# Optimization experiments

Hardware: AMD Instinct MI355X
Metric: run time of the kernel (lower is better)

Reference implementation:

```python
import jax, jax.numpy as jnp
import numpy as np

N_NODES = 200000
N_EDGES = 800000
N_GRAPHS = 4096
ATOM_DIM = 128
HIDDEN = 256
LN_EPS = 1e-5


def _layer_norm(x, g, b):
    m = jnp.mean(x, axis=-1, keepdims=True)
    v = jnp.mean((x - m) ** 2, axis=-1, keepdims=True)
    return (x - m) / jnp.sqrt(v + LN_EPS) * g + b


def setup_inputs() -> dict:
    key = jax.random.key(0)
    ks = jax.random.split(key, 16)
    d = {}
    d['x'] = jax.random.normal(ks[0], (N_NODES, ATOM_DIM), dtype=jnp.float32)
    d['edge_index'] = jax.random.randint(ks[1], (2, N_EDGES), 0, N_NODES, dtype=jnp.int32)
    # sorted batch assignment covering all graphs (PyG batches are sorted)
    d['batch'] = ((jnp.arange(N_NODES) * N_GRAPHS) // N_NODES).astype(jnp.int32)

    def glorot(k, shape):
        fan_in, fan_out = shape[0], shape[1]
        s = jnp.sqrt(2.0 / (fan_in + fan_out))
        return jax.random.normal(k, shape, dtype=jnp.float32) * s

    d['gin1_w1'] = glorot(ks[2], (ATOM_DIM, HIDDEN)); d['gin1_b1'] = jnp.zeros((HIDDEN,), jnp.float32)
    d['gin1_w2'] = glorot(ks[3], (HIDDEN, HIDDEN));  d['gin1_b2'] = jnp.zeros((HIDDEN,), jnp.float32)
    d['gin2_w1'] = glorot(ks[4], (HIDDEN, HIDDEN));  d['gin2_b1'] = jnp.zeros((HIDDEN,), jnp.float32)
    d['gin2_w2'] = glorot(ks[5], (HIDDEN, HIDDEN));  d['gin2_b2'] = jnp.zeros((HIDDEN,), jnp.float32)
    d['ln_g'] = jnp.ones((HIDDEN,), jnp.float32);    d['ln_b'] = jnp.zeros((HIDDEN,), jnp.float32)
    d['s2_w1'] = glorot(ks[6], (HIDDEN, 768));       d['s2_b1'] = jnp.zeros((768,), jnp.float32)
    d['s2_ln_g'] = jnp.ones((768,), jnp.float32);    d['s2_ln_b'] = jnp.zeros((768,), jnp.float32)
    d['s2_w2'] = glorot(ks[7], (768, 2));            d['s2_b2'] = jnp.zeros((2,), jnp.float32)
    return d


def reference(x, edge_index, batch,
              gin1_w1, gin1_b1, gin1_w2, gin1_b2,
              gin2_w1, gin2_b1, gin2_w2, gin2_b2,
              ln_g, ln_b,
              s2_w1, s2_b1, s2_ln_g, s2_ln_b, s2_w2, s2_b2):
    src, dst = edge_index[0], edge_index[1]

    def gin_conv(h, w1, b1, w2, b2):
        # GINConv: mlp((1+eps)*x + sum_{j in N(i)} x_j), eps=0
        agg = jax.ops.segment_sum(h[src], dst, num_segments=h.shape[0])
        z = h + agg
        return jax.nn.relu(z @ w1 + b1) @ w2 + b2

    h = gin_conv(x, gin1_w1, gin1_b1, gin1_w2, gin1_b2)
    h = jax.nn.leaky_relu(_layer_norm(h, ln_g, ln_b), 0.2)
    h = gin_conv(h, gin2_w1, gin2_b1, gin2_w2, gin2_b2)
    h = jax.nn.leaky_relu(h, 0.2)
    # global max pool over graphs
    g = jax.ops.segment_max(h, batch, num_segments=N_GRAPHS)
    # seq2 head (dropout = identity in eval)
    z = jax.nn.leaky_relu(_layer_norm(g @ s2_w1 + s2_b1, s2_ln_g, s2_ln_b), 0.2)
    z = z @ s2_w2 + s2_b2
    return jax.nn.softmax(z, axis=-1)
```

## Files before the change

### kernel.cpp

```cpp
#include <hip/hip_runtime.h>

#define NN 200000
#define NE 800000
#define NG 4096
#define AD 128
#define HD 256
#define LN_EPS 1e-5f
#define NB 782

typedef __attribute__((ext_vector_type(8))) short     bf16x8;
typedef __attribute__((ext_vector_type(8))) unsigned short us8;
typedef __attribute__((ext_vector_type(4))) unsigned short us4;
typedef __attribute__((ext_vector_type(4))) float     f32x4;

typedef __attribute__((address_space(1))) const unsigned gl_t;
typedef __attribute__((address_space(3))) unsigned       ld_t;

__device__ __forceinline__ float leaky(float v){ return v > 0.f ? v : 0.2f*v; }

__device__ __forceinline__ unsigned short f2bf(float f){
  unsigned u = __float_as_uint(f);
  return (unsigned short)((u + 0x7FFFu + ((u >> 16) & 1u)) >> 16);
}
__device__ __forceinline__ float bf2f(unsigned short h){ return __uint_as_float(((unsigned)h) << 16); }

__device__ __forceinline__ unsigned fkey(float f){
  unsigned u = __float_as_uint(f);
  return (u & 0x80000000u) ? ~u : (u | 0x80000000u);
}
__device__ __forceinline__ float fdec(unsigned k){
  return (k & 0x80000000u) ? __uint_as_float(k & 0x7FFFFFFFu) : __uint_as_float(~k);
}

__global__ __launch_bounds__(256) void k_zero(int* __restrict__ cur){
  int i = blockIdx.x * 256 + threadIdx.x;
  if (i < NN) cur[i] = 0;
}

__global__ __launch_bounds__(256) void k_count(const int* __restrict__ ei, int* __restrict__ cur){
  int e = blockIdx.x * 256 + threadIdx.x;
  atomicAdd(&cur[ei[NE + e]], 1);
}

__global__ __launch_bounds__(256) void k_scanA(const int* __restrict__ cur, int* __restrict__ partial){
  __shared__ int sd[256];
  int t = threadIdx.x, b = blockIdx.x, i = b * 256 + t;
  sd[t] = (i < NN) ? cur[i] : 0;
  __syncthreads();
  for (int off = 128; off >= 1; off >>= 1){
    if (t < off) sd[t] += sd[t + off];
    __syncthreads();
  }
  if (t == 0) partial[b] = sd[0];
}

__global__ __launch_bounds__(1024) void k_scanB(const int* __restrict__ partial,
                                                int* __restrict__ scanoff, int* __restrict__ rowptr){
  __shared__ int sd[1024];
  int t = threadIdx.x;
  int v = (t < NB) ? partial[t] : 0;
  sd[t] = v; __syncthreads();
  for (int off = 1; off < 1024; off <<= 1){
    int u = (t >= off) ? sd[t - off] : 0;
    __syncthreads();
    sd[t] += u;
    __syncthreads();
  }
  if (t < NB) scanoff[t] = sd[t] - v;
  if (t == 0) rowptr[NN] = NE;
}

__global__ __launch_bounds__(256) void k_scanC(int* __restrict__ cur, const int* __restrict__ scanoff,
                                               int* __restrict__ rowptr){
  __shared__ int sd[256];
  int t = threadIdx.x, b = blockIdx.x, i = b * 256 + t;
  int v = (i < NN) ? cur[i] : 0;
  sd[t] = v; __syncthreads();
  for (int off = 1; off < 256; off <<= 1){
    int u = (t >= off) ? sd[t - off] : 0;
    __syncthreads();
    sd[t] += u;
    __syncthreads();
  }
  if (i < NN){ rowptr[i] = scanoff[b] + sd[t] - v; cur[i] = 0; }
}

__global__ __launch_bounds__(256) void k_fill(const int* __restrict__ ei,
                                              const int* __restrict__ rowptr,
                                              int* __restrict__ cur,
                                              int* __restrict__ col){
  int e = blockIdx.x * 256 + threadIdx.x;
  int s = ei[e], d = ei[NE + e];
  int pos = atomicAdd(&cur[d], 1);
  col[rowptr[d] + pos] = s;
}

__global__ __launch_bounds__(256) void k_initG(unsigned* __restrict__ Gk){
  int i = blockIdx.x * 256 + threadIdx.x;
  Gk[i] = 0x00800000u;
}

__global__ __launch_bounds__(256) void k_wprep(const float* __restrict__ src,
                                               unsigned short* __restrict__ dst, int K){
  int k = blockIdx.x, n = threadIdx.x;
  dst[(size_t)n * K + k] = f2bf(src[(size_t)k * 256 + n]);
}

__global__ __launch_bounds__(256) void k_layer1(const float* __restrict__ x,
                                                const int* __restrict__ rowptr,
                                                const int* __restrict__ col,
                                                const unsigned short* __restrict__ W1T,
                                                const float* __restrict__ b1,
                                                const unsigned short* __restrict__ W2T,
                                                const float* __restrict__ b2,
                                                const float* __restrict__ lng,
                                                const float* __restrict__ lnb,
                                                unsigned short* __restrict__ H1){
  __shared__ alignas(16) char gbuf[32768 + 4096];
  __shared__ float2 redS[16][4];
  char* zS = gbuf + 32768;
  char* tS = gbuf;
  const int tid = threadIdx.x;
  const int l = tid & 63, wv = tid >> 6;
  const int cl = l & 15, kg = l >> 4;
  const int row0 = blockIdx.x * 16;
  const int r16 = tid >> 4, sub = tid & 15;
  const int grow = row0 + r16;

  const float4* x4 = (const float4*)x;
  float a[8];
  {
    float4 s0 = x4[(size_t)grow * 32 + sub * 2];
    float4 s1 = x4[(size_t)grow * 32 + sub * 2 + 1];
    a[0]=s0.x; a[1]=s0.y; a[2]=s0.z; a[3]=s0.w; a[4]=s1.x; a[5]=s1.y; a[6]=s1.z; a[7]=s1.w;
  }
  const int pr = rowptr[grow], per = rowptr[grow + 1];
  const int p0 = rowptr[row0], pend = rowptr[row0 + 16];

  for (int cs = p0; cs < pend; cs += 64){
    const int ns = min(64, pend - cs);
    {
      const int cidx = cs + wv * 16 + (l & 15);
      int colv = (cidx < pend) ? col[cidx] : 0;
      #pragma unroll
      for (int i = 0; i < 8; ++i){
        const int lslot = wv * 16 + i * 2 + (l >> 5);
        const int j = __shfl(colv, i * 2 + (l >> 5));
        if (lslot < ns){
          const void* src = (const void*)(x + (size_t)j * AD + (l & 31) * 4);
          void* dst = (void*)(gbuf + (wv * 16 + i * 2) * 512);
          __builtin_amdgcn_global_load_lds((gl_t*)src, (ld_t*)dst, 16, 0, 0);
        }
      }
    }
    __syncthreads();
    {
      const int qlo = max(pr, cs), qhi = min(per, cs + ns);
      for (int q = qlo; q < qhi; ++q){
        const float4* lrow = (const float4*)(gbuf + (q - cs) * 512 + sub * 32);
        float4 c0 = lrow[0], c1 = lrow[1];
        a[0]+=c0.x; a[1]+=c0.y; a[2]+=c0.z; a[3]+=c0.w;
        a[4]+=c1.x; a[5]+=c1.y; a[6]+=c1.z; a[7]+=c1.w;
      }
    }
    __syncthreads();
  }

  {
    us8 o;
    #pragma unroll
    for (int j = 0; j < 8; ++j) o[j] = f2bf(a[j]);
    *(us8*)&zS[r16 * 256 + ((sub * 16) ^ ((r16 & 7) << 4))] = o;
  }
  __syncthreads();

  f32x4 acc[4];
  #pragma unroll
  for (int nt = 0; nt < 4; ++nt){
    float bv = b1[wv * 64 + nt * 16 + cl];
    acc[nt] = (f32x4){bv, bv, bv, bv};
  }
  #pragma unroll
  for (int ks = 0; ks < 4; ++ks){
    const int kb = (ks * 32 + kg * 8) * 2;
    bf16x8 a0 = *(const bf16x8*)&zS[cl * 256 + (kb ^ ((cl & 7) << 4))];
    #pragma unroll
    for (int nt = 0; nt < 4; ++nt){
      bf16x8 b = *(const bf16x8*)(W1T + (size_t)(wv * 64 + nt * 16 + cl) * AD + ks * 32 + kg * 8);
      acc[nt] = __builtin_amdgcn_mfma_f32_16x16x32_bf16(a0, b, acc[nt], 0, 0, 0);
    }
  }
  #pragma unroll
  for (int nt = 0; nt < 4; ++nt)
    #pragma unroll
    for (int rg = 0; rg < 4; ++rg){
      float v = fmaxf(acc[nt][rg], 0.f);
      int row = kg * 4 + rg;
      int cc = wv * 64 + nt * 16 + cl;
      *(unsigned short*)&tS[row * 512 + ((cc * 2) ^ ((row & 7) << 4))] = f2bf(v);
    }
  __syncthreads();

  #pragma unroll
  for (int nt = 0; nt < 4; ++nt){
    float bv = b2[wv * 64 + nt * 16 + cl];
    acc[nt] = (f32x4){bv, bv, bv, bv};
  }
  #pragma unroll
  for (int ks = 0; ks < 8; ++ks){
    const int kb = (ks * 32 + kg * 8) * 2;
    bf16x8 a0 = *(const bf16x8*)&tS[cl * 512 + (kb ^ ((cl & 7) << 4))];
    #pragma unroll
    for (int nt = 0; nt < 4; ++nt){
      bf16x8 b = *(const bf16x8*)(W2T + (size_t)(wv * 64 + nt * 16 + cl) * HD + ks * 32 + kg * 8);
      acc[nt] = __builtin_amdgcn_mfma_f32_16x16x32_bf16(a0, b, acc[nt], 0, 0, 0);
    }
  }

  float s1v[4], s2v[4];
  #pragma unroll
  for (int rg = 0; rg < 4; ++rg){
    float aa = acc[0][rg] + acc[1][rg] + acc[2][rg] + acc[3][rg];
    float bb = acc[0][rg]*acc[0][rg] + acc[1][rg]*acc[1][rg]
             + acc[2][rg]*acc[2][rg] + acc[3][rg]*acc[3][rg];
    #pragma unroll
    for (int off = 1; off <= 8; off <<= 1){ aa += __shfl_xor(aa, off); bb += __shfl_xor(bb, off); }
    s1v[rg] = aa; s2v[rg] = bb;
  }
  if (cl == 0){
    #pragma unroll
    for (int rg = 0; rg < 4; ++rg)
      redS[kg * 4 + rg][wv] = make_float2(s1v[rg], s2v[rg]);
  }
  __syncthreads();
  #pragma unroll
  for (int rg = 0; rg < 4; ++rg){
    int row = kg * 4 + rg;
    float t1 = redS[row][0].x + redS[row][1].x + redS[row][2].x + redS[row][3].x;
    float t2 = redS[row][0].y + redS[row][1].y + redS[row][2].y + redS[row][3].y;
    float m  = t1 * (1.f / HD);
    float vr = t2 * (1.f / HD) - m * m;
    float rs = rsqrtf(vr + LN_EPS);
    #pragma unroll
    for (int nt = 0; nt < 4; ++nt){
      int cc = wv * 64 + nt * 16 + cl;
      float v = (acc[nt][rg] - m) * rs * lng[cc] + lnb[cc];
      H1[(size_t)(row0 + row) * HD + cc] = f2bf(leaky(v));
    }
  }
}

__global__ __launch_bounds__(256) void k_layer2(const unsigned short* __restrict__ H1,
                                                const int* __restrict__ rowptr,
                                                const int* __restrict__ col,
                                                const int* __restrict__ batch,
                                                const unsigned short* __restrict__ W1T,
                                                const float* __restrict__ b1,
                                                const unsigned short* __restrict__ W2T,
                                                const float* __restrict__ b2,
                                                unsigned* __restrict__ Gk){
  __shared__ alignas(16) char gbuf[32768 + 8192];
  char* zS = gbuf + 32768;
  char* tS = gbuf;
  float* stageF = (float*)gbuf;
  const int tid = threadIdx.x;
  const int l = tid & 63, wv = tid >> 6;
  const int cl = l & 15, kg = l >> 4;
  const int row0 = blockIdx.x * 16;
  const int r16 = tid >> 4, sub = tid & 15;
  const int grow = row0 + r16;

  float a[16];
  {
    us8 a0 = *(const us8*)(H1 + (size_t)grow * HD + sub * 16);
    us8 a1 = *(const us8*)(H1 + (size_t)grow * HD + sub * 16 + 8);
    #pragma unroll
    for (int j = 0; j < 8; ++j){ a[j] = bf2f(a0[j]); a[8 + j] = bf2f(a1[j]); }
  }
  const int pr = rowptr[grow], per = rowptr[grow + 1];
  const int p0 = rowptr[row0], pend = rowptr[row0 + 16];

  for (int cs = p0; cs < pend; cs += 64){
    const int ns = min(64, pend - cs);
    {
      const int cidx = cs + wv * 16 + (l & 15);
      int colv = (cidx < pend) ? col[cidx] : 0;
      #pragma unroll
      for (int i = 0; i < 8; ++i){
        const int lslot = wv * 16 + i * 2 + (l >> 5);
        const int j = __shfl(colv, i * 2 + (l >> 5));
        if (lslot < ns){
          const void* src = (const void*)(H1 + (size_t)j * HD + (l & 31) * 8);
          void* dst = (void*)(gbuf + (wv * 16 + i * 2) * 512);
          __builtin_amdgcn_global_load_lds((gl_t*)src, (ld_t*)dst, 16, 0, 0);
        }
      }
    }
    __syncthreads();
    {
      const int qlo = max(pr, cs), qhi = min(per, cs + ns);
      for (int q = qlo; q < qhi; ++q){
        const us8* lrow = (const us8*)(gbuf + (q - cs) * 512 + sub * 32);
        us8 c0 = lrow[0], c1 = lrow[1];
        #pragma unroll
        for (int j = 0; j < 8; ++j){ a[j] += bf2f(c0[j]); a[8 + j] += bf2f(c1[j]); }
      }
    }
    __syncthreads();
  }

  {
    us8 o0, o1;
    #pragma unroll
    for (int j = 0; j < 8; ++j){ o0[j] = f2bf(a[j]); o1[j] = f2bf(a[8 + j]); }
    const int swz = (r16 & 7) << 4;
    *(us8*)&zS[r16 * 512 + ((sub * 32) ^ swz)]      = o0;
    *(us8*)&zS[r16 * 512 + ((sub * 32 + 16) ^ swz)] = o1;
  }
  __syncthreads();

  f32x4 acc[4];
  #pragma unroll
  for (int nt = 0; nt < 4; ++nt){
    float bv = b1[wv * 64 + nt * 16 + cl];
    acc[nt] = (f32x4){bv, bv, bv, bv};
  }
  #pragma unroll
  for (int ks = 0; ks < 8; ++ks){
    const int kb = (ks * 32 + kg * 8) * 2;
    bf16x8 a0 = *(const bf16x8*)&zS[cl * 512 + (kb ^ ((cl & 7) << 4))];
    #pragma unroll
    for (int nt = 0; nt < 4; ++nt){
      bf16x8 b = *(const bf16x8*)(W1T + (size_t)(wv * 64 + nt * 16 + cl) * HD + ks * 32 + kg * 8);
      acc[nt] = __builtin_amdgcn_mfma_f32_16x16x32_bf16(a0, b, acc[nt], 0, 0, 0);
    }
  }
  #pragma unroll
  for (int nt = 0; nt < 4; ++nt)
    #pragma unroll
    for (int rg = 0; rg < 4; ++rg){
      float v = fmaxf(acc[nt][rg], 0.f);
      int row = kg * 4 + rg;
      int cc = wv * 64 + nt * 16 + cl;
      *(unsigned short*)&tS[row * 512 + ((cc * 2) ^ ((row & 7) << 4))] = f2bf(v);
    }
  __syncthreads();

  #pragma unroll
  for (int nt = 0; nt < 4; ++nt){
    float bv = b2[wv * 64 + nt * 16 + cl];
    acc[nt] = (f32x4){bv, bv, bv, bv};
  }
  #pragma unroll
  for (int ks = 0; ks < 8; ++ks){
    const int kb = (ks * 32 + kg * 8) * 2;
    bf16x8 a0 = *(const bf16x8*)&tS[cl * 512 + (kb ^ ((cl & 7) << 4))];
    #pragma unroll
    for (int nt = 0; nt < 4; ++nt){
      bf16x8 b = *(const bf16x8*)(W2T + (size_t)(wv * 64 + nt * 16 + cl) * HD + ks * 32 + kg * 8);
      acc[nt] = __builtin_amdgcn_mfma_f32_16x16x32_bf16(a0, b, acc[nt], 0, 0, 0);
    }
  }
  __syncthreads();

  #pragma unroll
  for (int nt = 0; nt < 4; ++nt)
    #pragma unroll
    for (int rg = 0; rg < 4; ++rg){
      int row = kg * 4 + rg;
      int cc = wv * 64 + nt * 16 + cl;
      stageF[row * HD + cc] = leaky(acc[nt][rg]);
    }
  __syncthreads();

  {
    const int c = tid;
    int gprev = batch[row0];
    float m = -3.4e38f;
    #pragma unroll
    for (int r = 0; r < 16; ++r){
      int g = batch[row0 + r];
      if (g != gprev){
        atomicMax(&Gk[(size_t)gprev * HD + c], fkey(m));
        m = -3.4e38f;
        gprev = g;
      }
      m = fmaxf(m, stageF[r * HD + c]);
    }
    atomicMax(&Gk[(size_t)gprev * HD + c], fkey(m));
  }
}

__global__ __launch_bounds__(256) void head_kernel(const unsigned* __restrict__ Gk,
                                                   const float* __restrict__ w1,
                                                   const float* __restrict__ b1,
                                                   const float* __restrict__ lng,
                                                   const float* __restrict__ lnb,
                                                   const float* __restrict__ w2,
                                                   const float* __restrict__ b2,
                                                   float* __restrict__ out){
  __shared__ float gs[8][256];
  __shared__ float redA[8][4], redB[8][4];
  const int tid = threadIdx.x;
  const int g0 = blockIdx.x * 8;
  #pragma unroll
  for (int q = 0; q < 8; ++q) gs[q][tid] = fdec(Gk[(size_t)(g0 + q) * 256 + tid]);
  __syncthreads();

  float z[8][3];
  #pragma unroll
  for (int j = 0; j < 3; ++j){
    const int c = tid + j * 256;
    float a[8];
    float bv = b1[c];
    #pragma unroll
    for (int q = 0; q < 8; ++q) a[q] = bv;
    #pragma unroll 8
    for (int k = 0; k < 256; ++k){
      float w = w1[(size_t)k * 768 + c];
      #pragma unroll
      for (int q = 0; q < 8; ++q) a[q] += gs[q][k] * w;
    }
    #pragma unroll
    for (int q = 0; q < 8; ++q) z[q][j] = a[q];
  }

  const int lane = tid & 63, wv = tid >> 6;
  float mean[8], rs[8];
  {
    float s1[8], s2[8];
    #pragma unroll
    for (int q = 0; q < 8; ++q){
      s1[q] = z[q][0] + z[q][1] + z[q][2];
      s2[q] = z[q][0]*z[q][0] + z[q][1]*z[q][1] + z[q][2]*z[q][2];
    }
    #pragma unroll
    for (int off = 32; off >= 1; off >>= 1){
      #pragma unroll
      for (int q = 0; q < 8; ++q){ s1[q] += __shfl_xor(s1[q], off); s2[q] += __shfl_xor(s2[q], off); }
    }
    if (lane == 0){
      #pragma unroll
      for (int q = 0; q < 8; ++q){ redA[q][wv] = s1[q]; redB[q][wv] = s2[q]; }
    }
    __syncthreads();
    #pragma unroll
    for (int q = 0; q < 8; ++q){
      float t1 = redA[q][0] + redA[q][1] + redA[q][2] + redA[q][3];
      float t2 = redB[q][0] + redB[q][1] + redB[q][2] + redB[q][3];
      float m = t1 * (1.f / 768.f);
      float v = t2 * (1.f / 768.f) - m * m;
      mean[q] = m; rs[q] = rsqrtf(v + LN_EPS);
    }
  }
  __syncthreads();

  float p0[8], p1[8];
  #pragma unroll
  for (int q = 0; q < 8; ++q){ p0[q] = 0.f; p1[q] = 0.f; }
  #pragma unroll
  for (int j = 0; j < 3; ++j){
    const int c = tid + j * 256;
    float gcol = lng[c], bcol = lnb[c];
    float wa = w2[2 * c], wb = w2[2 * c + 1];
    #pragma unroll
    for (int q = 0; q < 8; ++q){
      float zz = leaky((z[q][j] - mean[q]) * rs[q] * gcol + bcol);
      p0[q] += zz * wa; p1[q] += zz * wb;
    }
  }
  #pragma unroll
  for (int off = 32; off >= 1; off >>= 1){
    #pragma unroll
    for (int q = 0; q < 8; ++q){ p0[q] += __shfl_xor(p0[q], off); p1[q] += __shfl_xor(p1[q], off); }
  }
  if (lane == 0){
    #pragma unroll
    for (int q = 0; q < 8; ++q){ redA[q][wv] = p0[q]; redB[q][wv] = p1[q]; }
  }
  __syncthreads();
  if (tid < 8){
    int q = tid;
    float l0 = redA[q][0] + redA[q][1] + redA[q][2] + redA[q][3] + b2[0];
    float l1 = redB[q][0] + redB[q][1] + redB[q][2] + redB[q][3] + b2[1];
    float mm = fmaxf(l0, l1);
    float e0 = expf(l0 - mm), e1 = expf(l1 - mm);
    float inv = 1.f / (e0 + e1);
    out[(size_t)(g0 + q) * 2 + 0] = e0 * inv;
    out[(size_t)(g0 + q) * 2 + 1] = e1 * inv;
  }
}

extern "C" void kernel_launch(void* const* d_in, const int* in_sizes, int n_in,
                              void* d_out, int out_size, void* d_ws, size_t ws_size,
                              hipStream_t stream){
  const float* x     = (const float*)d_in[0];
  const int*   ei    = (const int*)  d_in[1];
  const int*   batch = (const int*)  d_in[2];
  const float* g1w1  = (const float*)d_in[3];
  const float* g1b1  = (const float*)d_in[4];
  const float* g1w2  = (const float*)d_in[5];
  const float* g1b2  = (const float*)d_in[6];
  const float* g2w1  = (const float*)d_in[7];
  const float* g2b1  = (const float*)d_in[8];
  const float* g2w2  = (const float*)d_in[9];
  const float* g2b2  = (const float*)d_in[10];
  const float* lng   = (const float*)d_in[11];
  const float* lnb   = (const float*)d_in[12];
  const float* s2w1  = (const float*)d_in[13];
  const float* s2b1  = (const float*)d_in[14];
  const float* s2lng = (const float*)d_in[15];
  const float* s2lnb = (const float*)d_in[16];
  const float* s2w2  = (const float*)d_in[17];
  const float* s2b2  = (const float*)d_in[18];
  float* out = (float*)d_out;

  char* ws = (char*)d_ws;
  int*            rowptr  = (int*)(ws + 0);
  int*            col     = (int*)(ws + 800032);
  unsigned*       Gk      = (unsigned*)(ws + 4000032);
  int*            cur     = (int*)Gk;
  unsigned short* W1T1    = (unsigned short*)(ws + 8194336);
  unsigned short* W2T1    = (unsigned short*)(ws + 8259872);
  unsigned short* W1T2    = (unsigned short*)(ws + 8390944);
  unsigned short* W2T2    = (unsigned short*)(ws + 8522016);
  int*            partial = (int*)(ws + 8653088);
  int*            scanoff = (int*)(ws + 8657184);
  unsigned short* H1      = (unsigned short*)(ws + 8661280);

  k_zero <<<(NN + 255) / 256, 256, 0, stream>>>(cur);
  k_count<<<NE / 256,         256, 0, stream>>>(ei, cur);
  k_scanA<<<NB,               256, 0, stream>>>(cur, partial);
  k_scanB<<<1,               1024, 0, stream>>>(partial, scanoff, rowptr);
  k_scanC<<<NB,               256, 0, stream>>>(cur, scanoff, rowptr);
  k_fill <<<NE / 256,         256, 0, stream>>>(ei, rowptr, cur, col);
  k_initG<<<NG * HD / 256,    256, 0, stream>>>(Gk);
  k_wprep<<<128, 256, 0, stream>>>(g1w1, W1T1, 128);
  k_wprep<<<256, 256, 0, stream>>>(g1w2, W2T1, 256);
  k_wprep<<<256, 256, 0, stream>>>(g2w1, W1T2, 256);
  k_wprep<<<256, 256, 0, stream>>>(g2w2, W2T2, 256);
  k_layer1<<<NN / 16, 256, 0, stream>>>(x, rowptr, col, W1T1, g1b1, W2T1, g1b2, lng, lnb, H1);
  k_layer2<<<NN / 16, 256, 0, stream>>>(H1, rowptr, col, batch, W1T2, g2b1, W2T2, g2b2, Gk);
  head_kernel<<<NG / 8, 256, 0, stream>>>(Gk, s2w1, s2b1, s2lng, s2lnb, s2w2, s2b2, out);
}
```

Baseline: 899.5 us.

## Quantize gathered node features to int8 with per-row scales

Adds a pre-pass that quantizes the input features to int8 with a per-row absmax scale. Layer 1 now writes its output as int8 plus per-row scales instead of bf16. Both neighbor-aggregation gathers then read 1-byte rows and dequantize in LDS, cutting gather bandwidth and LDS footprint. This trades accuracy for bandwidth: int8 with per-row scaling loses precision relative to bf16 and fp32. It also adds an extra pass over x.

```diff
diff --git a/kernel.cpp b/kernel.cpp
--- a/kernel.cpp
+++ b/kernel.cpp
@@ -8,10 +8,11 @@
 #define LN_EPS 1e-5f
 #define NB 782
 
-typedef __attribute__((ext_vector_type(8))) short     bf16x8;
-typedef __attribute__((ext_vector_type(8))) unsigned short us8;
-typedef __attribute__((ext_vector_type(4))) unsigned short us4;
-typedef __attribute__((ext_vector_type(4))) float     f32x4;
+typedef __attribute__((ext_vector_type(8)))  short          bf16x8;
+typedef __attribute__((ext_vector_type(8)))  unsigned short us8;
+typedef __attribute__((ext_vector_type(4)))  float          f32x4;
+typedef __attribute__((ext_vector_type(8)))  signed char    i8x8;
+typedef __attribute__((ext_vector_type(16))) signed char    i8x16;
 
 typedef __attribute__((address_space(1))) const unsigned gl_t;
 typedef __attribute__((address_space(3))) unsigned       ld_t;
@@ -30,6 +31,11 @@
 }
 __device__ __forceinline__ float fdec(unsigned k){
   return (k & 0x80000000u) ? __uint_as_float(k & 0x7FFFFFFFu) : __uint_as_float(~k);
+}
+
+__device__ __forceinline__ signed char q8(float v, float inv){
+  float t = rintf(fmaxf(-127.f, fminf(127.f, v * inv)));
+  return (signed char)(int)t;
 }
 
 __global__ __launch_bounds__(256) void k_zero(int* __restrict__ cur){
@@ -106,7 +112,32 @@
   dst[(size_t)n * K + k] = f2bf(src[(size_t)k * 256 + n]);
 }
 
+__global__ __launch_bounds__(256) void k_xprep8(const float* __restrict__ x,
+                                                signed char* __restrict__ X8,
+                                                float* __restrict__ Xscale){
+  const int tid = threadIdx.x;
+  const int r16 = tid >> 4, sub = tid & 15;
+  const int grow = blockIdx.x * 16 + r16;
+  const float4* x4 = (const float4*)x;
+  float4 v0 = x4[(size_t)grow * 32 + sub * 2];
+  float4 v1 = x4[(size_t)grow * 32 + sub * 2 + 1];
+  float f[8] = {v0.x, v0.y, v0.z, v0.w, v1.x, v1.y, v1.z, v1.w};
+  float am = 0.f;
+  #pragma unroll
+  for (int j = 0; j < 8; ++j) am = fmaxf(am, fabsf(f[j]));
+  #pragma unroll
+  for (int off = 1; off <= 8; off <<= 1) am = fmaxf(am, __shfl_xor(am, off));
+  float inv = (am > 0.f) ? 127.f / am : 0.f;
+  i8x8 o;
+  #pragma unroll
+  for (int j = 0; j < 8; ++j) o[j] = q8(f[j], inv);
+  *(i8x8*)(X8 + (size_t)grow * 128 + sub * 8) = o;
+  if (sub == 0) Xscale[grow] = am * (1.f / 127.f);
+}
+
 __global__ __launch_bounds__(256) void k_layer1(const float* __restrict__ x,
+                                                const signed char* __restrict__ X8,
+                                                const float* __restrict__ Xscale,
                                                 const int* __restrict__ rowptr,
                                                 const int* __restrict__ col,
                                                 const unsigned short* __restrict__ W1T,
@@ -115,11 +146,15 @@
                                                 const float* __restrict__ b2,
                                                 const float* __restrict__ lng,
                                                 const float* __restrict__ lnb,
-                                                unsigned short* __restrict__ H1){
-  __shared__ alignas(16) char gbuf[32768 + 4096];
+                                                signed char* __restrict__ H1q,
+                                                float* __restrict__ Hscale){
+  __shared__ alignas(16) char gbuf[16384];
   __shared__ float2 redS[16][4];
-  char* zS = gbuf + 32768;
-  char* tS = gbuf;
+  __shared__ float  amaxS[16][4];
+  __shared__ float  sscaleX[64];
+  char* zS = gbuf;
+  char* tS = gbuf + 4096;
+  char* qS = gbuf + 12288;
   const int tid = threadIdx.x;
   const int l = tid & 63, wv = tid >> 6;
   const int cl = l & 15, kg = l >> 4;
@@ -127,9 +162,9 @@
   const int r16 = tid >> 4, sub = tid & 15;
   const int grow = row0 + r16;
 
-  const float4* x4 = (const float4*)x;
   float a[8];
   {
+    const float4* x4 = (const float4*)x;
     float4 s0 = x4[(size_t)grow * 32 + sub * 2];
     float4 s1 = x4[(size_t)grow * 32 + sub * 2 + 1];
     a[0]=s0.x; a[1]=s0.y; a[2]=s0.z; a[3]=s0.w; a[4]=s1.x; a[5]=s1.y; a[6]=s1.z; a[7]=s1.w;
@@ -142,13 +177,14 @@
     {
       const int cidx = cs + wv * 16 + (l & 15);
       int colv = (cidx < pend) ? col[cidx] : 0;
+      if (l < 16 && cidx < pend) sscaleX[wv * 16 + l] = Xscale[colv];
       #pragma unroll
-      for (int i = 0; i < 8; ++i){
-        const int lslot = wv * 16 + i * 2 + (l >> 5);
-        const int j = __shfl(colv, i * 2 + (l >> 5));
+      for (int i = 0; i < 2; ++i){
+        const int lslot = wv * 16 + i * 8 + (l >> 3);
+        const int j = __shfl(colv, i * 8 + (l >> 3));
         if (lslot < ns){
-          const void* src = (const void*)(x + (size_t)j * AD + (l & 31) * 4);
-          void* dst = (void*)(gbuf + (wv * 16 + i * 2) * 512);
+          const void* src = (const void*)(X8 + (size_t)j * 128 + (l & 7) * 16);
+          void* dst = (void*)(gbuf + (wv * 16 + i * 8) * 128);
           __builtin_amdgcn_global_load_lds((gl_t*)src, (ld_t*)dst, 16, 0, 0);
         }
       }
@@ -157,10 +193,10 @@
     {
       const int qlo = max(pr, cs), qhi = min(per, cs + ns);
       for (int q = qlo; q < qhi; ++q){
-        const float4* lrow = (const float4*)(gbuf + (q - cs) * 512 + sub * 32);
-        float4 c0 = lrow[0], c1 = lrow[1];
-        a[0]+=c0.x; a[1]+=c0.y; a[2]+=c0.z; a[3]+=c0.w;
-        a[4]+=c1.x; a[5]+=c1.y; a[6]+=c1.z; a[7]+=c1.w;
+        float s = sscaleX[q - cs];
+        i8x8 c = *(const i8x8*)(gbuf + (q - cs) * 128 + sub * 8);
+        #pragma unroll
+        for (int j = 0; j < 8; ++j) a[j] += s * (float)c[j];
       }
     }
     __syncthreads();
@@ -233,6 +269,9 @@
       redS[kg * 4 + rg][wv] = make_float2(s1v[rg], s2v[rg]);
   }
   __syncthreads();
+
+  float vout[4][4];
+  float amax_l[4];
   #pragma unroll
   for (int rg = 0; rg < 4; ++rg){
     int row = kg * 4 + rg;
@@ -241,16 +280,47 @@
     float m  = t1 * (1.f / HD);
     float vr = t2 * (1.f / HD) - m * m;
     float rs = rsqrtf(vr + LN_EPS);
+    float am = 0.f;
     #pragma unroll
     for (int nt = 0; nt < 4; ++nt){
       int cc = wv * 64 + nt * 16 + cl;
-      float v = (acc[nt][rg] - m) * rs * lng[cc] + lnb[cc];
-      H1[(size_t)(row0 + row) * HD + cc] = f2bf(leaky(v));
-    }
-  }
-}
-
-__global__ __launch_bounds__(256) void k_layer2(const unsigned short* __restrict__ H1,
+      float v = leaky((acc[nt][rg] - m) * rs * lng[cc] + lnb[cc]);
+      vout[rg][nt] = v;
+      am = fmaxf(am, fabsf(v));
+    }
+    #pragma unroll
+    for (int off = 1; off <= 8; off <<= 1) am = fmaxf(am, __shfl_xor(am, off));
+    amax_l[rg] = am;
+  }
+  if (cl == 0){
+    #pragma unroll
+    for (int rg = 0; rg < 4; ++rg)
+      amaxS[kg * 4 + rg][wv] = amax_l[rg];
+  }
+  __syncthreads();
+
+  #pragma unroll
+  for (int rg = 0; rg < 4; ++rg){
+    int row = kg * 4 + rg;
+    float am = fmaxf(fmaxf(amaxS[row][0], amaxS[row][1]), fmaxf(amaxS[row][2], amaxS[row][3]));
+    float inv = (am > 0.f) ? 127.f / am : 0.f;
+    #pragma unroll
+    for (int nt = 0; nt < 4; ++nt){
+      int cc = wv * 64 + nt * 16 + cl;
+      qS[row * 256 + cc] = (char)q8(vout[rg][nt], inv);
+    }
+    if (wv == 0 && cl == 0) Hscale[row0 + row] = am * (1.f / 127.f);
+  }
+  __syncthreads();
+
+  {
+    int r = tid >> 4, off = (tid & 15) * 16;
+    *(int4*)(H1q + (size_t)(row0 + r) * 256 + off) = *(const int4*)&qS[r * 256 + off];
+  }
+}
+
+__global__ __launch_bounds__(256) void k_layer2(const signed char* __restrict__ H1q,
+                                                const float* __restrict__ Hscale,
                                                 const int* __restrict__ rowptr,
                                                 const int* __restrict__ col,
                                                 const int* __restrict__ batch,
@@ -259,9 +329,10 @@
                                                 const unsigned short* __restrict__ W2T,
                                                 const float* __restrict__ b2,
                                                 unsigned* __restrict__ Gk){
-  __shared__ alignas(16) char gbuf[32768 + 8192];
-  char* zS = gbuf + 32768;
-  char* tS = gbuf;
+  __shared__ alignas(16) char gbuf[16384];
+  __shared__ float sscaleH[64];
+  char* zS = gbuf;
+  char* tS = gbuf + 8192;
   float* stageF = (float*)gbuf;
   const int tid = threadIdx.x;
   const int l = tid & 63, wv = tid >> 6;
@@ -272,10 +343,10 @@
 
   float a[16];
   {
-    us8 a0 = *(const us8*)(H1 + (size_t)grow * HD + sub * 16);
-    us8 a1 = *(const us8*)(H1 + (size_t)grow * HD + sub * 16 + 8);
-    #pragma unroll
-    for (int j = 0; j < 8; ++j){ a[j] = bf2f(a0[j]); a[8 + j] = bf2f(a1[j]); }
+    float s = Hscale[grow];
+    i8x16 c = *(const i8x16*)(H1q + (size_t)grow * 256 + sub * 16);
+    #pragma unroll
+    for (int j = 0; j < 16; ++j) a[j] = s * (float)c[j];
   }
   const int pr = rowptr[grow], per = rowptr[grow + 1];
   const int p0 = rowptr[row0], pend = rowptr[row0 + 16];
@@ -285,13 +356,14 @@
     {
       const int cidx = cs + wv * 16 + (l & 15);
       int colv = (cidx < pend) ? col[cidx] : 0;
+      if (l < 16 && cidx < pend) sscaleH[wv * 16 + l] = Hscale[colv];
       #pragma unroll
-      for (int i = 0; i < 8; ++i){
-        const int lslot = wv * 16 + i * 2 + (l >> 5);
-        const int j = __shfl(colv, i * 2 + (l >> 5));
+      for (int i = 0; i < 4; ++i){
+        const int lslot = wv * 16 + i * 4 + (l >> 4);
+        const int j = __shfl(colv, i * 4 + (l >> 4));
         if (lslot < ns){
-          const void* src = (const void*)(H1 + (size_t)j * HD + (l & 31) * 8);
-          void* dst = (void*)(gbuf + (wv * 16 + i * 2) * 512);
+          const void* src = (const void*)(H1q + (size_t)j * 256 + (l & 15) * 16);
+          void* dst = (void*)(gbuf + (wv * 16 + i * 4) * 256);
           __builtin_amdgcn_global_load_lds((gl_t*)src, (ld_t*)dst, 16, 0, 0);
         }
       }
@@ -300,10 +372,10 @@
     {
       const int qlo = max(pr, cs), qhi = min(per, cs + ns);
       for (int q = qlo; q < qhi; ++q){
-        const us8* lrow = (const us8*)(gbuf + (q - cs) * 512 + sub * 32);
-        us8 c0 = lrow[0], c1 = lrow[1];
+        float s = sscaleH[q - cs];
+        i8x16 c = *(const i8x16*)(gbuf + (q - cs) * 256 + sub * 16);
         #pragma unroll
-        for (int j = 0; j < 8; ++j){ a[j] += bf2f(c0[j]); a[8 + j] += bf2f(c1[j]); }
+        for (int j = 0; j < 16; ++j) a[j] += s * (float)c[j];
       }
     }
     __syncthreads();
@@ -526,20 +598,26 @@
   unsigned short* W2T2    = (unsigned short*)(ws + 8522016);
   int*            partial = (int*)(ws + 8653088);
   int*            scanoff = (int*)(ws + 8657184);
-  unsigned short* H1      = (unsigned short*)(ws + 8661280);
-
-  k_zero <<<(NN + 255) / 256, 256, 0, stream>>>(cur);
-  k_count<<<NE / 256,         256, 0, stream>>>(ei, cur);
-  k_scanA<<<NB,               256, 0, stream>>>(cur, partial);
-  k_scanB<<<1,               1024, 0, stream>>>(partial, scanoff, rowptr);
-  k_scanC<<<NB,               256, 0, stream>>>(cur, scanoff, rowptr);
-  k_fill <<<NE / 256,         256, 0, stream>>>(ei, rowptr, cur, col);
-  k_initG<<<NG * HD / 256,    256, 0, stream>>>(Gk);
-  k_wprep<<<128, 256, 0, stream>>>(g1w1, W1T1, 128);
-  k_wprep<<<256, 256, 0, stream>>>(g1w2, W2T1, 256);
-  k_wprep<<<256, 256, 0, stream>>>(g2w1, W1T2, 256);
-  k_wprep<<<256, 256, 0, stream>>>(g2w2, W2T2, 256);
-  k_layer1<<<NN / 16, 256, 0, stream>>>(x, rowptr, col, W1T1, g1b1, W2T1, g1b2, lng, lnb, H1);
-  k_layer2<<<NN / 16, 256, 0, stream>>>(H1, rowptr, col, batch, W1T2, g2b1, W2T2, g2b2, Gk);
+  signed char*    H1q     = (signed char*)(ws + 8661280);
+  float*          Hscale  = (float*)(ws + 59861280);
+  signed char*    X8      = (signed char*)(ws + 60661280);
+  float*          Xscale  = (float*)(ws + 86261280);
+
+  k_zero  <<<(NN + 255) / 256, 256, 0, stream>>>(cur);
+  k_count <<<NE / 256,         256, 0, stream>>>(ei, cur);
+  k_scanA <<<NB,               256, 0, stream>>>(cur, partial);
+  k_scanB <<<1,               1024, 0, stream>>>(partial, scanoff, rowptr);
+  k_scanC <<<NB,               256, 0, stream>>>(cur, scanoff, rowptr);
+  k_fill  <<<NE / 256,         256, 0, stream>>>(ei, rowptr, cur, col);
+  k_initG <<<NG * HD / 256,    256, 0, stream>>>(Gk);
+  k_wprep <<<128, 256, 0, stream>>>(g1w1, W1T1, 128);
+  k_wprep <<<256, 256, 0, stream>>>(g1w2, W2T1, 256);
+  k_wprep <<<256, 256, 0, stream>>>(g2w1, W1T2, 256);
+  k_wprep <<<256, 256, 0, stream>>>(g2w2, W2T2, 256);
+  k_xprep8<<<NN / 16,          256, 0, stream>>>(x, X8, Xscale);
+  k_layer1<<<NN / 16, 256, 0, stream>>>(x, X8, Xscale, rowptr, col,
+                                        W1T1, g1b1, W2T1, g1b2, lng, lnb, H1q, Hscale);
+  k_layer2<<<NN / 16, 256, 0, stream>>>(H1q, Hscale, rowptr, col, batch,
+                                        W1T2, g2b1, W2T2, g2b2, Gk);
   head_kernel<<<NG / 8, 256, 0, stream>>>(Gk, s2w1, s2b1, s2lng, s2lnb, s2w2, s2b2, out);
 }
```

Result: no change. 914.4 us (+1.7%).
